# Kernel optimization log

Hardware: AMD Instinct MI355X
Metric: run time of the kernel (lower is better)

## Reference

```python
import jax, jax.numpy as jnp
import numpy as np

N = 65536          # nodes per snapshot
B = 32             # batch
COMP = 2           # components (u, v)
SFC = 2            # number of space-filling-curve orderings
K, S, P = 32, 4, 16  # dimension==2 branch: kernel, stride, padding
CHANNELS = [2, 4, 8, 16, 16, 16]  # per-layer channels (x2 until num_final_channels=16)
NCONV = 5          # conv sizes: 65536->16385->4097->1025->257->65
FINAL_SIZE = 65


def _neigh_idx(n):
    # get_neighbourhood_md(arange(n), gen_neighbour_keys(1), ordering=True):
    # per-node [i-1, i, i+1], clamped at boundaries.
    i = jnp.arange(n)
    return jnp.stack([jnp.clip(i - 1, 0, n - 1), i, jnp.clip(i + 1, 0, n - 1)], axis=-1)


def setup_inputs() -> dict:
    key = jax.random.key(0)
    ks = jax.random.split(key, 16)
    d = {}
    d["x"] = jax.random.normal(ks[0], (B, N, COMP), jnp.float32)
    d["orderings"] = jax.random.randint(ks[1], (SFC, N), 0, N)  # SFC permutations (gather indices)
    d["sp_w"] = jnp.ones((N, 3), jnp.float32) / 3.0  # NearestNeighbouring weights (shared over sfcs)
    d["sp_b"] = jnp.zeros((N,), jnp.float32)
    for j in range(NCONV):
        cin, cout = CHANNELS[j], CHANNELS[j + 1]
        d[f"conv_w{j}"] = jax.random.normal(ks[2 + j], (cout, cin, K), jnp.float32) * (1.0 / np.sqrt(cin * K))
        d[f"conv_b{j}"] = jnp.zeros((cout,), jnp.float32)
    fc_in = SFC * CHANNELS[-1] * FINAL_SIZE  # 2080
    d["fc1_w"] = jax.random.normal(ks[8], (128, fc_in), jnp.float32) * (1.0 / np.sqrt(fc_in))
    d["fc1_b"] = jnp.zeros((128,), jnp.float32)
    d["fc2_w"] = jax.random.normal(ks[9], (16, 128), jnp.float32) * (1.0 / np.sqrt(128))
    d["fc2_b"] = jnp.zeros((16,), jnp.float32)
    return d


def _forward(x, orderings, sp_w, sp_b, conv_ws, conv_bs, fc1_w, fc1_b, fc2_w, fc2_b):
    neigh = _neigh_idx(N)  # (N,3)
    feats = []
    for i in range(SFC):
        a = x[:, orderings[i], :]            # SFC permutation gather -> (B,N,C)
        a = jnp.transpose(a, (0, 2, 1))      # (B,C,N)
        g = a[:, :, neigh]                   # neighbourhood gather -> (B,C,N,3)
        a = jnp.tanh(jnp.einsum('bcnk,nk->bcn', g, sp_w) + sp_b)  # sparse NN combine
        for w, b in zip(conv_ws, conv_bs):
            a = jax.lax.conv_general_dilated(a, w, (S,), [(P, P)],
                                             dimension_numbers=('NCH', 'OIH', 'NCH'))
            a = jnp.tanh(a + b[None, :, None])
        feats.append(a.reshape(a.shape[0], -1))  # (B, 16*65)
    h = jnp.concatenate(feats, axis=-1)          # (B, 2080)
    h = jnp.tanh(h @ fc1_w.T + fc1_b)            # (B, 128)
    h = jnp.tanh(h @ fc2_w.T + fc2_b)            # (B, 16) latent
    return h


def reference(x, orderings, sp_w, sp_b, conv_w0, conv_b0, conv_w1, conv_b1, conv_w2, conv_b2,
              conv_w3, conv_b3, conv_w4, conv_b4, fc1_w, fc1_b, fc2_w, fc2_b):
    conv_ws = [conv_w0, conv_w1, conv_w2, conv_w3, conv_w4]
    conv_bs = [conv_b0, conv_b1, conv_b2, conv_b3, conv_b4]
    return _forward(x, orderings, sp_w, sp_b, conv_ws, conv_bs, fc1_w, fc1_b, fc2_w, fc2_b)
```

## Files before the change

kernel.cpp:

```cpp
#include <hip/hip_runtime.h>
#include <math.h>

#define NPTS 65536

__device__ __forceinline__ float4 ld4_guard(const float* __restrict__ row, int pos, int hi) {
    float4 v;
    if (pos >= 0 && pos + 4 <= hi) {
        v = *(const float4*)(row + pos);
    } else {
        v.x = (pos + 0 >= 0 && pos + 0 < hi) ? row[pos + 0] : 0.f;
        v.y = (pos + 1 >= 0 && pos + 1 < hi) ? row[pos + 1] : 0.f;
        v.z = (pos + 2 >= 0 && pos + 2 < hi) ? row[pos + 2] : 0.f;
        v.w = (pos + 3 >= 0 && pos + 3 < hi) ? row[pos + 3] : 0.f;
    }
    return v;
}

__device__ __forceinline__ int pmap(int p) { return p + ((p >> 5) << 2); }
__device__ __forceinline__ int pm8(int p) { return p + ((p >> 3) << 2); }

__global__ __launch_bounds__(256) void transpose_kernel(const float* __restrict__ x,
                                                        float* __restrict__ xt)
{
    __shared__ float tile[64][65];
    int n0 = blockIdx.x * 64;
    int tid = threadIdx.x;
    int lane = tid & 63, w = tid >> 6;
    const float2* x2 = (const float2*)x;
#pragma unroll
    for (int bq = 0; bq < 8; ++bq) {
        int b = bq * 4 + w;
        float2 v = x2[(size_t)b * NPTS + n0 + lane];
        tile[lane][b * 2 + 0] = v.x;
        tile[lane][b * 2 + 1] = v.y;
    }
    __syncthreads();
    int f4 = tid & 15;
#pragma unroll
    for (int rq = 0; rq < 4; ++rq) {
        int r = rq * 16 + (tid >> 4);
        float4 v = make_float4(tile[r][f4 * 4 + 0], tile[r][f4 * 4 + 1],
                               tile[r][f4 * 4 + 2], tile[r][f4 * 4 + 3]);
        *(float4*)&xt[(size_t)(n0 + r) * 64 + f4 * 4] = v;
    }
}

__global__ __launch_bounds__(256) void smooth_kernel(const float* __restrict__ xt,
                                                     const int* __restrict__ ord,
                                                     const float* __restrict__ sp_w,
                                                     const float* __restrict__ sp_b,
                                                     float* __restrict__ s)
{
    __shared__ int s_idx[130];
    __shared__ float rows[130][65];
    int n0 = blockIdx.x * 128;
    int tid = threadIdx.x;
    if (tid < 130) {
        int g = n0 - 1 + tid;
        g = g < 0 ? 0 : (g > NPTS - 1 ? NPTS - 1 : g);
        s_idx[tid] = ord[g];
    }
    __syncthreads();
    for (int q = tid; q < 130 * 16; q += 256) {
        int r = q >> 4, f4 = q & 15;
        float4 v = *(const float4*)&xt[(size_t)s_idx[r] * 64 + f4 * 4];
        rows[r][f4 * 4 + 0] = v.x; rows[r][f4 * 4 + 1] = v.y;
        rows[r][f4 * 4 + 2] = v.z; rows[r][f4 * 4 + 3] = v.w;
    }
    __syncthreads();
    int n_local = tid & 127, half = tid >> 7;
    int n = n0 + n_local;
    float w0 = sp_w[n * 3 + 0], w1 = sp_w[n * 3 + 1], w2 = sp_w[n * 3 + 2];
    float bb = sp_b[n];
#pragma unroll 4
    for (int bc = 0; bc < 64; bc += 2) {
        int bce = bc + half;
        float v = w0 * rows[n_local][bce] + w1 * rows[n_local + 1][bce]
                + w2 * rows[n_local + 2][bce] + bb;
        s[(size_t)bce * NPTS + n] = tanhf(v);
    }
}

__global__ __launch_bounds__(256, 2) void conv0_wpc(
    const float* __restrict__ in,
    const float* __restrict__ w,
    const float* __restrict__ bias,
    float* __restrict__ out)
{
    constexpr int SPAN = 2076;
    __shared__ float in_s[2][2336];

    int bid = blockIdx.x;
    int tile = bid % 33;
    int b = bid / 33;
    int tid = threadIdx.x;

    int base = tile * 2048 - 16;
    const float* inb = in + (size_t)b * 2 * NPTS;
    for (int q = tid; q < 2 * (SPAN / 4); q += 256) {
        int ci = q / (SPAN / 4), fp = q - ci * (SPAN / 4);
        int p = 4 * fp;
        float4 v = ld4_guard(inb + (size_t)ci * NPTS, base + p, NPTS);
        *(float4*)&in_s[ci][pmap(p)] = v;
    }
    __syncthreads();

    int lane = tid & 63;
    int co_u = __builtin_amdgcn_readfirstlane(tid >> 6);

    float acc[8];
    float bv = bias[co_u];
#pragma unroll
    for (int j = 0; j < 8; ++j) acc[j] = bv;

#pragma unroll 1
    for (int ci = 0; ci < 2; ++ci) {
        const float* wb = w + (co_u * 2 + ci) * 32;
        float wv[32];
#pragma unroll
        for (int k = 0; k < 32; ++k) wv[k] = wb[k];
        float4 v[15];
#pragma unroll
        for (int k = 0; k < 15; ++k)
            v[k] = *(const float4*)&in_s[ci][pmap(32 * lane + 4 * k)];
#pragma unroll
        for (int k4 = 0; k4 < 8; ++k4) {
            float wx = wv[4 * k4], wy = wv[4 * k4 + 1], wz = wv[4 * k4 + 2], ww = wv[4 * k4 + 3];
#pragma unroll
            for (int j = 0; j < 8; ++j)
                acc[j] += v[j + k4].x * wx + v[j + k4].y * wy
                        + v[j + k4].z * wz + v[j + k4].w * ww;
        }
    }

    int l0 = tile * 512 + lane * 8;
    size_t row = ((size_t)b * 4 + co_u) * 16388;
    if (l0 + 8 <= 16385) {
        float4 s0 = make_float4(tanhf(acc[0]), tanhf(acc[1]), tanhf(acc[2]), tanhf(acc[3]));
        float4 s1 = make_float4(tanhf(acc[4]), tanhf(acc[5]), tanhf(acc[6]), tanhf(acc[7]));
        *(float4*)&out[row + l0] = s0;
        *(float4*)&out[row + l0 + 4] = s1;
    } else {
#pragma unroll
        for (int j = 0; j < 8; ++j)
            if (l0 + j < 16385) out[row + l0 + j] = tanhf(acc[j]);
    }
}

__global__ __launch_bounds__(512) void conv1_wpc(
    const float* __restrict__ in,
    const float* __restrict__ w,
    const float* __restrict__ bias,
    float* __restrict__ out)
{
    constexpr int SPAN = 1052;
    __shared__ float in_s[4][1184];

    int bid = blockIdx.x;
    int tile = bid % 17;
    int b = bid / 17;
    int tid = threadIdx.x;

    int base = tile * 1024 - 16;
    const float* inb = in + (size_t)b * 4 * 16388;
    for (int q = tid; q < 4 * (SPAN / 4); q += 512) {
        int ci = q / (SPAN / 4), fp = q - ci * (SPAN / 4);
        int p = 4 * fp;
        float4 v = ld4_guard(inb + (size_t)ci * 16388, base + p, 16385);
        *(float4*)&in_s[ci][pmap(p)] = v;
    }
    __syncthreads();

    int lane = tid & 63;
    int co_u = __builtin_amdgcn_readfirstlane(tid >> 6);

    float acc[4];
    float bv = bias[co_u];
#pragma unroll
    for (int j = 0; j < 4; ++j) acc[j] = bv;

#pragma unroll 1
    for (int ci = 0; ci < 4; ++ci) {
        const float* wb = w + (co_u * 4 + ci) * 32;
        float wv[32];
#pragma unroll
        for (int k = 0; k < 32; ++k) wv[k] = wb[k];
        float4 v[11];
#pragma unroll
        for (int k = 0; k < 11; ++k)
            v[k] = *(const float4*)&in_s[ci][pmap(16 * lane + 4 * k)];
#pragma unroll
        for (int k4 = 0; k4 < 8; ++k4) {
            float wx = wv[4 * k4], wy = wv[4 * k4 + 1], wz = wv[4 * k4 + 2], ww = wv[4 * k4 + 3];
#pragma unroll
            for (int j = 0; j < 4; ++j)
                acc[j] += v[j + k4].x * wx + v[j + k4].y * wy
                        + v[j + k4].z * wz + v[j + k4].w * ww;
        }
    }

    int l0 = tile * 256 + lane * 4;
    size_t row = ((size_t)b * 8 + co_u) * 4100;
    if (l0 + 4 <= 4097) {
        float4 s0 = make_float4(tanhf(acc[0]), tanhf(acc[1]), tanhf(acc[2]), tanhf(acc[3]));
        *(float4*)&out[row + l0] = s0;
    } else {
#pragma unroll
        for (int j = 0; j < 4; ++j)
            if (l0 + j < 4097) out[row + l0 + j] = tanhf(acc[j]);
    }
}

__global__ __launch_bounds__(512) void conv23_kernel(
    const float* __restrict__ c1,
    const float* __restrict__ w2, const float* __restrict__ b2,
    const float* __restrict__ w3, const float* __restrict__ b3,
    float* __restrict__ c3out)
{
    __shared__ __align__(16) float st[8][760];
    __shared__ __align__(16) float c2s[16][236];

    int b = blockIdx.x >> 3;
    int t = blockIdx.x & 7;
    int tid = threadIdx.x;
    int lane = tid & 63;
    int co_u = __builtin_amdgcn_readfirstlane(tid >> 6);

    int l3_0 = t * 33;
    int s2 = 4 * l3_0 - 16;
    int s1 = 4 * s2 - 16;

    const float* c1b = c1 + (size_t)b * 8 * 4100;
    for (int q = tid; q < 8 * 167; q += 512) {
        int ci = q / 167, p4 = q - ci * 167;
        float4 v = ld4_guard(c1b + (size_t)ci * 4100, s1 + 4 * p4, 4097);
        *(float4*)&st[ci][pmap(4 * p4)] = v;
    }
    __syncthreads();

    {
        int i0 = 3 * lane;
        if (i0 < 160) {
            float acc[2][3];
            float ba = b2[co_u], bb = b2[co_u + 8];
#pragma unroll
            for (int j = 0; j < 3; ++j) { acc[0][j] = ba; acc[1][j] = bb; }
#pragma unroll 1
            for (int ci = 0; ci < 8; ++ci) {
                const float* wa = w2 + (size_t)(co_u * 8 + ci) * 32;
                const float* wb = w2 + (size_t)((co_u + 8) * 8 + ci) * 32;
                float4 v[10];
#pragma unroll
                for (int k = 0; k < 10; ++k)
                    v[k] = *(const float4*)&st[ci][pmap(12 * lane + 4 * k)];
#pragma unroll
                for (int k4 = 0; k4 < 8; ++k4) {
                    float4 wva = *(const float4*)(wa + 4 * k4);
                    float4 wvb = *(const float4*)(wb + 4 * k4);
#pragma unroll
                    for (int j = 0; j < 3; ++j) {
                        acc[0][j] += v[k4 + j].x * wva.x + v[k4 + j].y * wva.y
                                   + v[k4 + j].z * wva.z + v[k4 + j].w * wva.w;
                        acc[1][j] += v[k4 + j].x * wvb.x + v[k4 + j].y * wvb.y
                                   + v[k4 + j].z * wvb.z + v[k4 + j].w * wvb.w;
                    }
                }
            }
#pragma unroll
            for (int j = 0; j < 3; ++j) {
                int i = i0 + j;
                if (i < 160) {
                    int l2 = s2 + i;
                    bool val = (l2 >= 0) && (l2 < 1025);
                    c2s[co_u][pm8(i)]     = val ? tanhf(acc[0][j]) : 0.f;
                    c2s[co_u + 8][pm8(i)] = val ? tanhf(acc[1][j]) : 0.f;
                }
            }
        }
    }
    __syncthreads();

    if (lane < 33) {
        int l3 = l3_0 + lane;
        if (l3 < 257) {
            float acc0 = b3[co_u], acc1 = b3[co_u + 8];
#pragma unroll 1
            for (int ci = 0; ci < 16; ++ci) {
                const float* wa = w3 + (size_t)(co_u * 16 + ci) * 32;
                const float* wb = w3 + (size_t)((co_u + 8) * 16 + ci) * 32;
                float4 v[8];
#pragma unroll
                for (int k = 0; k < 8; ++k)
                    v[k] = *(const float4*)&c2s[ci][pm8(4 * lane + 4 * k)];
#pragma unroll
                for (int k4 = 0; k4 < 8; ++k4) {
                    float4 wva = *(const float4*)(wa + 4 * k4);
                    float4 wvb = *(const float4*)(wb + 4 * k4);
                    acc0 += v[k4].x * wva.x + v[k4].y * wva.y
                          + v[k4].z * wva.z + v[k4].w * wva.w;
                    acc1 += v[k4].x * wvb.x + v[k4].y * wvb.y
                          + v[k4].z * wvb.z + v[k4].w * wvb.w;
                }
            }
            c3out[((size_t)b * 16 + co_u) * 260 + l3] = tanhf(acc0);
            c3out[((size_t)b * 16 + co_u + 8) * 260 + l3] = tanhf(acc1);
        }
    }
}

__global__ __launch_bounds__(256) void conv4_kernel(
    const float* __restrict__ c3,
    const float* __restrict__ w4, const float* __restrict__ b4,
    float* __restrict__ feats, int ibase)
{
    __shared__ __align__(16) float st[16][320];
    __shared__ float w4s[8][16][32];
    int b = blockIdx.x >> 1, h = blockIdx.x & 1;
    int tid = threadIdx.x;
    for (int i = tid; i < 8 * 16 * 32; i += 256) ((float*)w4s)[i] = w4[h * 4096 + i];
    const float* c3b = c3 + (size_t)b * 16 * 260;
    for (int q = tid; q < 16 * 72; q += 256) {
        int ci = q / 72, p4 = q - ci * 72;
        float4 v = ld4_guard(c3b + (size_t)ci * 260, 4 * p4 - 16, 257);
        *(float4*)&st[ci][pmap(4 * p4)] = v;
    }
    __syncthreads();
    for (int q = tid; q < 520; q += 256) {
        int co_l = q / 65, l4 = q - co_l * 65;
        int co = h * 8 + co_l;
        float acc = b4[co];
#pragma unroll 1
        for (int ci = 0; ci < 16; ++ci) {
#pragma unroll
            for (int k4 = 0; k4 < 8; ++k4) {
                float4 v = *(const float4*)&st[ci][pmap(4 * l4 + 4 * k4)];
                const float* wk = &w4s[co_l][ci][4 * k4];
                acc += v.x * wk[0] + v.y * wk[1] + v.z * wk[2] + v.w * wk[3];
            }
        }
        feats[(size_t)(b & 31) * 2080 + (size_t)((b >> 5) + ibase) * 1040 + co * 65 + l4]
            = tanhf(acc);
    }
}

__global__ __launch_bounds__(256) void fc1_kernel(const float* __restrict__ h,
                                                  const float* __restrict__ w,
                                                  const float* __restrict__ bias,
                                                  float* __restrict__ out)
{
    int lane = threadIdx.x & 63;
    int wid = blockIdx.x * 4 + (threadIdx.x >> 6);
#pragma unroll
    for (int r = 0; r < 4; ++r) {
        int o = wid + r * 1024;
        int b = o >> 7, j = o & 127;
        const float4* h4 = (const float4*)(h + (size_t)b * 2080);
        const float4* w4 = (const float4*)(w + (size_t)j * 2080);
        float acc = 0.f;
#pragma unroll
        for (int q = 0; q < 8; ++q) {
            float4 a = h4[lane + 64 * q], c = w4[lane + 64 * q];
            acc += a.x * c.x + a.y * c.y + a.z * c.z + a.w * c.w;
        }
        if (lane < 8) {
            float4 a = h4[512 + lane], c = w4[512 + lane];
            acc += a.x * c.x + a.y * c.y + a.z * c.z + a.w * c.w;
        }
        for (int off = 32; off; off >>= 1) acc += __shfl_down(acc, off, 64);
        if (lane == 0) out[b * 128 + j] = tanhf(acc + bias[j]);
    }
}

__global__ __launch_bounds__(256) void fc2_kernel(const float* __restrict__ h,
                                                  const float* __restrict__ w,
                                                  const float* __restrict__ bias,
                                                  float* __restrict__ out)
{
    int lane = threadIdx.x & 63;
    int o = blockIdx.x * 4 + (threadIdx.x >> 6);
    int b = o >> 4, j = o & 15;
    const float* hb = h + (size_t)b * 128;
    const float* wj = w + (size_t)j * 128;
    float acc = hb[lane] * wj[lane] + hb[lane + 64] * wj[lane + 64];
    for (int off = 32; off; off >>= 1) acc += __shfl_down(acc, off, 64);
    if (lane == 0) out[o] = tanhf(acc + bias[j]);
}

extern "C" void kernel_launch(void* const* d_in, const int* in_sizes, int n_in,
                              void* d_out, int out_size, void* d_ws, size_t ws_size,
                              hipStream_t stream)
{
    const float* x = (const float*)d_in[0];
    const int* orderings = (const int*)d_in[1];
    const float* sp_w = (const float*)d_in[2];
    const float* sp_b = (const float*)d_in[3];
    const float* conv_w[5];
    const float* conv_b[5];
    for (int j = 0; j < 5; ++j) {
        conv_w[j] = (const float*)d_in[4 + 2 * j];
        conv_b[j] = (const float*)d_in[5 + 2 * j];
    }
    const float* fc1_w = (const float*)d_in[14];
    const float* fc1_b = (const float*)d_in[15];
    const float* fc2_w = (const float*)d_in[16];
    const float* fc2_b = (const float*)d_in[17];

    float* ws = (float*)d_ws;

    if (ws_size >= 12583936ull * 4ull) {
        size_t o_xt = 0, o_c0 = 0, o_s = 4195328;
        size_t o_c1 = 4195328, o_c3 = 6294528, o_f = 6560768, o_h1 = 6627328;

        transpose_kernel<<<NPTS / 64, 256, 0, stream>>>(x, ws + o_xt);
        smooth_kernel<<<512, 256, 0, stream>>>(ws + o_xt, orderings, sp_w, sp_b, ws + o_s);
        smooth_kernel<<<512, 256, 0, stream>>>(ws + o_xt, orderings + NPTS, sp_w, sp_b,
                                               ws + o_s + 4194304);

        conv0_wpc<<<64 * 33, 256, 0, stream>>>(ws + o_s, conv_w[0], conv_b[0], ws + o_c0);
        conv1_wpc<<<64 * 17, 512, 0, stream>>>(ws + o_c0, conv_w[1], conv_b[1], ws + o_c1);
        conv23_kernel<<<64 * 8, 512, 0, stream>>>(ws + o_c1, conv_w[2], conv_b[2],
                                                  conv_w[3], conv_b[3], ws + o_c3);
        conv4_kernel<<<128, 256, 0, stream>>>(ws + o_c3, conv_w[4], conv_b[4],
                                              ws + o_f, 0);
        fc1_kernel<<<256, 256, 0, stream>>>(ws + o_f, fc1_w, fc1_b, ws + o_h1);
        fc2_kernel<<<128, 256, 0, stream>>>(ws + o_h1, fc2_w, fc2_b, (float*)d_out);
    } else {
        size_t o_xt = 0, o_s = 4194304, o_c0 = 8388608;
        size_t o_c1 = 4194304, o_c3 = 5243904, o_f = 10486272, o_h1 = 10552832;

        transpose_kernel<<<NPTS / 64, 256, 0, stream>>>(x, ws + o_xt);
        for (int i = 0; i < 2; ++i) {
            smooth_kernel<<<512, 256, 0, stream>>>(ws + o_xt, orderings + (size_t)i * NPTS,
                                                   sp_w, sp_b, ws + o_s);
            conv0_wpc<<<32 * 33, 256, 0, stream>>>(ws + o_s, conv_w[0], conv_b[0], ws + o_c0);
            conv1_wpc<<<32 * 17, 512, 0, stream>>>(ws + o_c0, conv_w[1], conv_b[1], ws + o_c1);
            conv23_kernel<<<32 * 8, 512, 0, stream>>>(ws + o_c1, conv_w[2], conv_b[2],
                                                      conv_w[3], conv_b[3], ws + o_c3);
            conv4_kernel<<<64, 256, 0, stream>>>(ws + o_c3, conv_w[4], conv_b[4],
                                                 ws + o_f, i);
        }
        fc1_kernel<<<256, 256, 0, stream>>>(ws + o_f, fc1_w, fc1_b, ws + o_h1);
        fc2_kernel<<<128, 256, 0, stream>>>(ws + o_h1, fc2_w, fc2_b, (float*)d_out);
    }
}
```

Before: 150.8 us.

## Split fused conv2/conv3 kernel into separate per-layer conv kernels

Replaces the fused conv23 kernel, which recomputed overlapping conv2 halos per tile in shared memory, with two separate kernels. conv2 writes its full output to a global workspace buffer, and conv3 reads it back. This removes the redundant halo recompute and the idle lanes in the fused kernel, and gives each layer a tiling that fits its size. In exchange it adds one kernel launch and a global round trip for the conv2 activations.

Result: faster. 138.7 us (-8.0%).

```diff
diff --git a/kernel.cpp b/kernel.cpp
--- a/kernel.cpp
+++ b/kernel.cpp
@@ -17,7 +17,6 @@
 }
 
 __device__ __forceinline__ int pmap(int p) { return p + ((p >> 5) << 2); }
-__device__ __forceinline__ int pm8(int p) { return p + ((p >> 3) << 2); }
 
 __global__ __launch_bounds__(256) void transpose_kernel(const float* __restrict__ x,
                                                         float* __restrict__ xt)
@@ -211,100 +210,126 @@
     }
 }
 
-__global__ __launch_bounds__(512) void conv23_kernel(
-    const float* __restrict__ c1,
-    const float* __restrict__ w2, const float* __restrict__ b2,
-    const float* __restrict__ w3, const float* __restrict__ b3,
-    float* __restrict__ c3out)
-{
-    __shared__ __align__(16) float st[8][760];
-    __shared__ __align__(16) float c2s[16][236];
-
-    int b = blockIdx.x >> 3;
-    int t = blockIdx.x & 7;
-    int tid = threadIdx.x;
+__global__ __launch_bounds__(512) void conv2_wpc(
+    const float* __restrict__ in,
+    const float* __restrict__ w,
+    const float* __restrict__ bias,
+    float* __restrict__ out)
+{
+    constexpr int SPAN = 540;
+    __shared__ float in_s[8][608];
+
+    int bid = blockIdx.x;
+    int tile = bid % 9;
+    int b = bid / 9;
+    int tid = threadIdx.x;
+
+    int base = tile * 512 - 16;
+    const float* inb = in + (size_t)b * 8 * 4100;
+    for (int q = tid; q < 8 * (SPAN / 4); q += 512) {
+        int ci = q / (SPAN / 4), fp = q - ci * (SPAN / 4);
+        int p = 4 * fp;
+        float4 v = ld4_guard(inb + (size_t)ci * 4100, base + p, 4097);
+        *(float4*)&in_s[ci][pmap(p)] = v;
+    }
+    __syncthreads();
+
     int lane = tid & 63;
     int co_u = __builtin_amdgcn_readfirstlane(tid >> 6);
 
-    int l3_0 = t * 33;
-    int s2 = 4 * l3_0 - 16;
-    int s1 = 4 * s2 - 16;
-
-    const float* c1b = c1 + (size_t)b * 8 * 4100;
-    for (int q = tid; q < 8 * 167; q += 512) {
-        int ci = q / 167, p4 = q - ci * 167;
-        float4 v = ld4_guard(c1b + (size_t)ci * 4100, s1 + 4 * p4, 4097);
-        *(float4*)&st[ci][pmap(4 * p4)] = v;
-    }
-    __syncthreads();
-
-    {
-        int i0 = 3 * lane;
-        if (i0 < 160) {
-            float acc[2][3];
-            float ba = b2[co_u], bb = b2[co_u + 8];
-#pragma unroll
-            for (int j = 0; j < 3; ++j) { acc[0][j] = ba; acc[1][j] = bb; }
+    float acc[2][2];
+    acc[0][0] = acc[0][1] = bias[co_u];
+    acc[1][0] = acc[1][1] = bias[co_u + 8];
+
 #pragma unroll 1
-            for (int ci = 0; ci < 8; ++ci) {
-                const float* wa = w2 + (size_t)(co_u * 8 + ci) * 32;
-                const float* wb = w2 + (size_t)((co_u + 8) * 8 + ci) * 32;
-                float4 v[10];
-#pragma unroll
-                for (int k = 0; k < 10; ++k)
-                    v[k] = *(const float4*)&st[ci][pmap(12 * lane + 4 * k)];
-#pragma unroll
-                for (int k4 = 0; k4 < 8; ++k4) {
-                    float4 wva = *(const float4*)(wa + 4 * k4);
-                    float4 wvb = *(const float4*)(wb + 4 * k4);
-#pragma unroll
-                    for (int j = 0; j < 3; ++j) {
-                        acc[0][j] += v[k4 + j].x * wva.x + v[k4 + j].y * wva.y
-                                   + v[k4 + j].z * wva.z + v[k4 + j].w * wva.w;
-                        acc[1][j] += v[k4 + j].x * wvb.x + v[k4 + j].y * wvb.y
-                                   + v[k4 + j].z * wvb.z + v[k4 + j].w * wvb.w;
-                    }
-                }
+    for (int ci = 0; ci < 8; ++ci) {
+        const float* wa = w + (size_t)(co_u * 8 + ci) * 32;
+        const float* wb = w + (size_t)((co_u + 8) * 8 + ci) * 32;
+        float4 v[9];
+#pragma unroll
+        for (int k = 0; k < 9; ++k)
+            v[k] = *(const float4*)&in_s[ci][pmap(8 * lane + 4 * k)];
+#pragma unroll
+        for (int k4 = 0; k4 < 8; ++k4) {
+            float4 wva = *(const float4*)(wa + 4 * k4);
+            float4 wvb = *(const float4*)(wb + 4 * k4);
+#pragma unroll
+            for (int j = 0; j < 2; ++j) {
+                acc[0][j] += v[k4 + j].x * wva.x + v[k4 + j].y * wva.y
+                           + v[k4 + j].z * wva.z + v[k4 + j].w * wva.w;
+                acc[1][j] += v[k4 + j].x * wvb.x + v[k4 + j].y * wvb.y
+                           + v[k4 + j].z * wvb.z + v[k4 + j].w * wvb.w;
             }
-#pragma unroll
-            for (int j = 0; j < 3; ++j) {
-                int i = i0 + j;
-                if (i < 160) {
-                    int l2 = s2 + i;
-                    bool val = (l2 >= 0) && (l2 < 1025);
-                    c2s[co_u][pm8(i)]     = val ? tanhf(acc[0][j]) : 0.f;
-                    c2s[co_u + 8][pm8(i)] = val ? tanhf(acc[1][j]) : 0.f;
-                }
-            }
-        }
-    }
-    __syncthreads();
-
-    if (lane < 33) {
-        int l3 = l3_0 + lane;
-        if (l3 < 257) {
-            float acc0 = b3[co_u], acc1 = b3[co_u + 8];
+        }
+    }
+
+    int l0 = tile * 128 + lane * 2;
+#pragma unroll
+    for (int h = 0; h < 2; ++h) {
+        size_t row = ((size_t)b * 16 + co_u + 8 * h) * 1028;
+        if (l0 + 2 <= 1025) {
+            float2 st2 = make_float2(tanhf(acc[h][0]), tanhf(acc[h][1]));
+            *(float2*)&out[row + l0] = st2;
+        } else {
+#pragma unroll
+            for (int j = 0; j < 2; ++j)
+                if (l0 + j < 1025) out[row + l0 + j] = tanhf(acc[h][j]);
+        }
+    }
+}
+
+__global__ __launch_bounds__(512) void conv3_wpc(
+    const float* __restrict__ in,
+    const float* __restrict__ w,
+    const float* __restrict__ bias,
+    float* __restrict__ out)
+{
+    constexpr int SPAN = 284;
+    __shared__ float in_s[16][320];
+
+    int bid = blockIdx.x;
+    int tile = bid % 5;
+    int b = bid / 5;
+    int tid = threadIdx.x;
+
+    int base = tile * 256 - 16;
+    const float* inb = in + (size_t)b * 16 * 1028;
+    for (int q = tid; q < 16 * (SPAN / 4); q += 512) {
+        int ci = q / (SPAN / 4), fp = q - ci * (SPAN / 4);
+        int p = 4 * fp;
+        float4 v = ld4_guard(inb + (size_t)ci * 1028, base + p, 1025);
+        *(float4*)&in_s[ci][pmap(p)] = v;
+    }
+    __syncthreads();
+
+    int lane = tid & 63;
+    int co_u = __builtin_amdgcn_readfirstlane(tid >> 6);
+
+    float acc0 = bias[co_u], acc1 = bias[co_u + 8];
+
 #pragma unroll 1
-            for (int ci = 0; ci < 16; ++ci) {
-                const float* wa = w3 + (size_t)(co_u * 16 + ci) * 32;
-                const float* wb = w3 + (size_t)((co_u + 8) * 16 + ci) * 32;
-                float4 v[8];
-#pragma unroll
-                for (int k = 0; k < 8; ++k)
-                    v[k] = *(const float4*)&c2s[ci][pm8(4 * lane + 4 * k)];
-#pragma unroll
-                for (int k4 = 0; k4 < 8; ++k4) {
-                    float4 wva = *(const float4*)(wa + 4 * k4);
-                    float4 wvb = *(const float4*)(wb + 4 * k4);
-                    acc0 += v[k4].x * wva.x + v[k4].y * wva.y
-                          + v[k4].z * wva.z + v[k4].w * wva.w;
-                    acc1 += v[k4].x * wvb.x + v[k4].y * wvb.y
-                          + v[k4].z * wvb.z + v[k4].w * wvb.w;
-                }
-            }
-            c3out[((size_t)b * 16 + co_u) * 260 + l3] = tanhf(acc0);
-            c3out[((size_t)b * 16 + co_u + 8) * 260 + l3] = tanhf(acc1);
-        }
+    for (int ci = 0; ci < 16; ++ci) {
+        const float* wa = w + (size_t)(co_u * 16 + ci) * 32;
+        const float* wb = w + (size_t)((co_u + 8) * 16 + ci) * 32;
+        float4 v[8];
+#pragma unroll
+        for (int k = 0; k < 8; ++k)
+            v[k] = *(const float4*)&in_s[ci][pmap(4 * lane + 4 * k)];
+#pragma unroll
+        for (int k4 = 0; k4 < 8; ++k4) {
+            float4 wva = *(const float4*)(wa + 4 * k4);
+            float4 wvb = *(const float4*)(wb + 4 * k4);
+            acc0 += v[k4].x * wva.x + v[k4].y * wva.y
+                  + v[k4].z * wva.z + v[k4].w * wva.w;
+            acc1 += v[k4].x * wvb.x + v[k4].y * wvb.y
+                  + v[k4].z * wvb.z + v[k4].w * wvb.w;
+        }
+    }
+
+    int l3 = tile * 64 + lane;
+    if (l3 < 257) {
+        out[((size_t)b * 16 + co_u) * 260 + l3] = tanhf(acc0);
+        out[((size_t)b * 16 + co_u + 8) * 260 + l3] = tanhf(acc1);
     }
 }
 
@@ -409,7 +434,8 @@
 
     if (ws_size >= 12583936ull * 4ull) {
         size_t o_xt = 0, o_c0 = 0, o_s = 4195328;
-        size_t o_c1 = 4195328, o_c3 = 6294528, o_f = 6560768, o_h1 = 6627328;
+        size_t o_c1 = 4195328, o_c2 = 6294528, o_c3 = 7347200;
+        size_t o_f = 7613440, o_h1 = 7680000;
 
         transpose_kernel<<<NPTS / 64, 256, 0, stream>>>(x, ws + o_xt);
         smooth_kernel<<<512, 256, 0, stream>>>(ws + o_xt, orderings, sp_w, sp_b, ws + o_s);
@@ -418,15 +444,16 @@
 
         conv0_wpc<<<64 * 33, 256, 0, stream>>>(ws + o_s, conv_w[0], conv_b[0], ws + o_c0);
         conv1_wpc<<<64 * 17, 512, 0, stream>>>(ws + o_c0, conv_w[1], conv_b[1], ws + o_c1);
-        conv23_kernel<<<64 * 8, 512, 0, stream>>>(ws + o_c1, conv_w[2], conv_b[2],
-                                                  conv_w[3], conv_b[3], ws + o_c3);
+        conv2_wpc<<<64 * 9, 512, 0, stream>>>(ws + o_c1, conv_w[2], conv_b[2], ws + o_c2);
+        conv3_wpc<<<64 * 5, 512, 0, stream>>>(ws + o_c2, conv_w[3], conv_b[3], ws + o_c3);
         conv4_kernel<<<128, 256, 0, stream>>>(ws + o_c3, conv_w[4], conv_b[4],
                                               ws + o_f, 0);
         fc1_kernel<<<256, 256, 0, stream>>>(ws + o_f, fc1_w, fc1_b, ws + o_h1);
         fc2_kernel<<<128, 256, 0, stream>>>(ws + o_h1, fc2_w, fc2_b, (float*)d_out);
     } else {
         size_t o_xt = 0, o_s = 4194304, o_c0 = 8388608;
-        size_t o_c1 = 4194304, o_c3 = 5243904, o_f = 10486272, o_h1 = 10552832;
+        size_t o_c1 = 4194304, o_c2 = 5243904, o_c3 = 5770240;
+        size_t o_f = 10486272, o_h1 = 10552832;
 
         transpose_kernel<<<NPTS / 64, 256, 0, stream>>>(x, ws + o_xt);
         for (int i = 0; i < 2; ++i) {
@@ -434,8 +461,8 @@
                                                    sp_w, sp_b, ws + o_s);
             conv0_wpc<<<32 * 33, 256, 0, stream>>>(ws + o_s, conv_w[0], conv_b[0], ws + o_c0);
             conv1_wpc<<<32 * 17, 512, 0, stream>>>(ws + o_c0, conv_w[1], conv_b[1], ws + o_c1);
-            conv23_kernel<<<32 * 8, 512, 0, stream>>>(ws + o_c1, conv_w[2], conv_b[2],
-                                                      conv_w[3], conv_b[3], ws + o_c3);
+            conv2_wpc<<<32 * 9, 512, 0, stream>>>(ws + o_c1, conv_w[2], conv_b[2], ws + o_c2);
+            conv3_wpc<<<32 * 5, 512, 0, stream>>>(ws + o_c2, conv_w[3], conv_b[3], ws + o_c3);
             conv4_kernel<<<64, 256, 0, stream>>>(ws + o_c3, conv_w[4], conv_b[4],
                                                  ws + o_f, i);
         }
```
